# Performance work log

Hardware: AMD Instinct MI355X
Metric: run time of the kernel (lower is better)

The kernel has to match this reference:

```python
import jax, jax.numpy as jnp
import numpy as np

EPS = 1e-5  # BatchNorm eps (torch default)


def point_sample(feat, points):
    """Bilinear sample feat [B,C,Hf,Wf] at points [B,K,2] (x,y in [0,1]),
    matching F.grid_sample(2*p-1, mode='bilinear', padding_mode='zeros',
    align_corners=False)."""
    B, C, Hf, Wf = feat.shape
    x = points[..., 0] * Wf - 0.5  # [B,K] pixel coords
    y = points[..., 1] * Hf - 0.5
    x0f = jnp.floor(x); y0f = jnp.floor(y)
    wx = (x - x0f)[:, None, :]  # [B,1,K]
    wy = (y - y0f)[:, None, :]
    x0 = x0f.astype(jnp.int32); y0 = y0f.astype(jnp.int32)
    flat = feat.reshape(B, C, Hf * Wf)

    def gather(xi, yi):
        valid = ((xi >= 0) & (xi < Wf) & (yi >= 0) & (yi < Hf))[:, None, :]
        lin = jnp.clip(yi, 0, Hf - 1) * Wf + jnp.clip(xi, 0, Wf - 1)  # [B,K]
        idx = jnp.broadcast_to(lin[:, None, :], (B, C, lin.shape[1]))
        return jnp.take_along_axis(flat, idx, axis=2) * valid

    v00 = gather(x0, y0)
    v10 = gather(x0 + 1, y0)
    v01 = gather(x0, y0 + 1)
    v11 = gather(x0 + 1, y0 + 1)
    return (v00 * (1 - wx) * (1 - wy) + v10 * wx * (1 - wy)
            + v01 * (1 - wx) * wy + v11 * wx * wy)


def bn(x, g, b, m, v):
    # eval-mode BatchNorm1d over channel dim of [B,C,K]
    scale = (g / jnp.sqrt(v + EPS))[None, :, None]
    return (x - m[None, :, None]) * scale + b[None, :, None]


def setup_inputs() -> dict:
    key = jax.random.key(0)
    ks = jax.random.split(key, 20)
    B, H, W = 8, 512, 512
    Cf = 256
    d = {
        'uncertainty_map': jax.random.normal(ks[0], (B, 1, H, W), jnp.float32),
        'prev_mask': jax.random.uniform(ks[1], (B, 1, H, W), jnp.float32),
        'enc_f': jax.random.normal(ks[2], (B, Cf, 128, 128), jnp.float32),
        'w1': jax.random.normal(ks[3], (256, Cf + 1), jnp.float32) * 0.05,
        'b1': jax.random.normal(ks[4], (256,), jnp.float32) * 0.05,
        'g1': jnp.ones((256,), jnp.float32),
        'be1': jnp.zeros((256,), jnp.float32),
        'm1': jax.random.normal(ks[5], (256,), jnp.float32) * 0.1,
        'v1': jax.random.uniform(ks[6], (256,), jnp.float32) + 0.5,
        'w2': jax.random.normal(ks[7], (256, 256), jnp.float32) * 0.05,
        'b2': jax.random.normal(ks[8], (256,), jnp.float32) * 0.05,
        'g2': jnp.ones((256,), jnp.float32),
        'be2': jnp.zeros((256,), jnp.float32),
        'm2': jax.random.normal(ks[9], (256,), jnp.float32) * 0.1,
        'v2': jax.random.uniform(ks[10], (256,), jnp.float32) + 0.5,
        'w3': jax.random.normal(ks[11], (1, 256), jnp.float32) * 0.05,
        'b3': jax.random.normal(ks[12], (1,), jnp.float32) * 0.05,
    }
    return d


def reference(uncertainty_map, prev_mask, enc_f,
              w1, b1, g1, be1, m1, v1,
              w2, b2, g2, be2, m2, v2,
              w3, b3):
    B, C, H, W = prev_mask.shape
    K = H * W // 10
    # K least-uncertain points (topk largest=False)
    _, idx = jax.lax.top_k(-uncertainty_map.reshape(B, -1), K)  # [B,K] int32
    col = (idx % W).astype(jnp.float32)
    row = (idx // W).astype(jnp.float32)
    points = jnp.stack([(col + 0.5) / W, (row + 0.5) / H], axis=-1)  # [B,K,2]

    coarse = point_sample(prev_mask, points)  # [B,1,K]
    fine = point_sample(enc_f, points)        # [B,Cf,K]
    h = jnp.concatenate([coarse, fine], axis=1)  # [B,Cf+1,K]

    h = jax.nn.relu(bn(jnp.einsum('oc,bck->bok', w1, h) + b1[None, :, None], g1, be1, m1, v1))
    h = jax.nn.relu(bn(jnp.einsum('oc,bck->bok', w2, h) + b2[None, :, None], g2, be2, m2, v2))
    refined = jax.nn.sigmoid(jnp.einsum('oc,bck->bok', w3, h) + b3[None, :, None])  # [B,1,K]

    flat = prev_mask.reshape(B, C, H * W)
    bi = jnp.arange(B)[:, None, None]
    ci = jnp.arange(C)[None, :, None]
    out = flat.at[bi, ci, idx[:, None, :]].set(jnp.broadcast_to(refined, (B, C, K)))
    return out.reshape(B, C, H, W)
```

## Files before the change

kernel.cpp:

```cpp
#include <hip/hip_runtime.h>
#include <hip/hip_bf16.h>

#define HW_IMG 262144
#define KSEL   26214
#define NB     8
#define CF     256
#define LDW1   288
#define LDACT  296
#define GBLK   410
#define MBLK   205
#define NPTS_PAD 26240

#define ACOL(c) ((c) ^ ((((c) >> 6) & 3) << 4))

typedef short    short8 __attribute__((ext_vector_type(8)));
typedef float    f32x4  __attribute__((ext_vector_type(4)));
typedef unsigned u32x2  __attribute__((ext_vector_type(2)));
typedef unsigned short u16x4 __attribute__((ext_vector_type(4)));

__device__ __forceinline__ unsigned f2key(float f){
    unsigned u = __builtin_bit_cast(unsigned, f);
    return (u & 0x80000000u) ? ~u : (u | 0x80000000u);
}
__device__ __forceinline__ unsigned short f2bf(float f){
    unsigned u = __builtin_bit_cast(unsigned, f);
    u = u + 0x7FFFu + ((u >> 16) & 1u);
    return (unsigned short)(u >> 16);
}
__device__ __forceinline__ float bf2f(unsigned short s){
    unsigned u = ((unsigned)s) << 16;
    return __builtin_bit_cast(float, u);
}

__global__ __launch_bounds__(256) void k_prep(
    const float* __restrict__ w1, const float* __restrict__ w2,
    const float* __restrict__ b1, const float* __restrict__ g1, const float* __restrict__ be1,
    const float* __restrict__ m1, const float* __restrict__ v1,
    const float* __restrict__ b2, const float* __restrict__ g2, const float* __restrict__ be2,
    const float* __restrict__ m2, const float* __restrict__ v2,
    unsigned short* __restrict__ w1p, unsigned short* __restrict__ w2p,
    float* __restrict__ c1, float* __restrict__ c2)
{
    int tid = blockIdx.x * 256 + threadIdx.x;
    if (tid < 256 * LDW1) {
        int o = tid / LDW1, k = tid % LDW1;
        float scale = g1[o] * rsqrtf(v1[o] + 1e-5f);
        float val = 0.f;
        if (k < 256) val = w1[o * 257 + k + 1];
        else if (k == 256) val = w1[o * 257];
        w1p[tid] = f2bf(val * scale);
        if (k == 0) c1[o] = (b1[o] - m1[o]) * scale + be1[o];
    } else {
        int t2 = tid - 256 * LDW1;
        if (t2 < 65536) {
            int o = t2 >> 8;
            float scale = g2[o] * rsqrtf(v2[o] + 1e-5f);
            w2p[t2] = f2bf(w2[t2] * scale);
            if ((t2 & 255) == 0) c2[o] = (b2[o] - m2[o]) * scale + be2[o];
        }
    }
}

__global__ __launch_bounds__(256) void k_transpose(
    const float* __restrict__ enc, unsigned short* __restrict__ encT)
{
    __shared__ __align__(16) unsigned short tile[64][72];
    int b = blockIdx.z;
    int pixbase = blockIdx.x * 64;
    int chbase  = blockIdx.y * 64;
    int t = threadIdx.x;
    int pix = t & 63, cg = t >> 6;
    const float* src = enc + (size_t)b * CF * 16384;
#pragma unroll
    for (int i = 0; i < 16; i++) {
        int c = chbase + cg * 16 + i;
        tile[pix][cg * 16 + i] = f2bf(src[(size_t)c * 16384 + pixbase + pix]);
    }
    __syncthreads();
    unsigned short* dst = encT + (size_t)b * 16384 * CF;
#pragma unroll
    for (int pass = 0; pass < 4; pass++) {
        int pl = pass * 16 + (t >> 4);
        int c4 = (t & 15) * 4;
        *(u16x4*)(dst + (size_t)(pixbase + pl) * CF + chbase + c4) = *(const u16x4*)&tile[pl][c4];
    }
}


__global__ __launch_bounds__(256) void k_histA(const float* __restrict__ unc, unsigned* __restrict__ hist)
{
    __shared__ unsigned lh[4][4096];
    int b = blockIdx.y, t = threadIdx.x;
    int wv = t >> 6;
    for (int i = t; i < 4 * 4096; i += 256) ((unsigned*)lh)[i] = 0;
    __syncthreads();
    const float4* src = (const float4*)(unc + (size_t)b * HW_IMG + blockIdx.x * 4096);
    unsigned* mine = lh[wv];
#pragma unroll
    for (int j = 0; j < 4; j++) {
        float4 v = src[j * 256 + t];
        atomicAdd(&mine[f2key(v.x) >> 20], 1u);
        atomicAdd(&mine[f2key(v.y) >> 20], 1u);
        atomicAdd(&mine[f2key(v.z) >> 20], 1u);
        atomicAdd(&mine[f2key(v.w) >> 20], 1u);
    }
    __syncthreads();
    unsigned* gh = hist + (size_t)b * 4096;
    for (int i = t; i < 4096; i += 256) {
        unsigned c = lh[0][i] + lh[1][i] + lh[2][i] + lh[3][i];
        if (c) atomicAdd(&gh[i], c);
    }
}

__global__ __launch_bounds__(256) void k_histB(const float* __restrict__ unc,
    const unsigned* __restrict__ meta, unsigned* __restrict__ hist)
{
    __shared__ unsigned lh[4096];
    int b = blockIdx.y, t = threadIdx.x;
    unsigned binA = meta[b * 8 + 0];
    for (int i = t; i < 4096; i += 256) lh[i] = 0;
    __syncthreads();
    const float4* src = (const float4*)(unc + (size_t)b * HW_IMG + blockIdx.x * 4096);
#pragma unroll
    for (int j = 0; j < 4; j++) {
        float4 v = src[j * 256 + t];
        unsigned k;
        k = f2key(v.x); if ((k >> 20) == binA) atomicAdd(&lh[(k >> 8) & 0xFFFu], 1u);
        k = f2key(v.y); if ((k >> 20) == binA) atomicAdd(&lh[(k >> 8) & 0xFFFu], 1u);
        k = f2key(v.z); if ((k >> 20) == binA) atomicAdd(&lh[(k >> 8) & 0xFFFu], 1u);
        k = f2key(v.w); if ((k >> 20) == binA) atomicAdd(&lh[(k >> 8) & 0xFFFu], 1u);
    }
    __syncthreads();
    unsigned* gh = hist + (size_t)b * 4096;
    for (int i = t; i < 4096; i += 256) { unsigned c = lh[i]; if (c) atomicAdd(&gh[i], c); }
}

__global__ __launch_bounds__(256) void k_histC(const float* __restrict__ unc,
    const unsigned* __restrict__ meta, unsigned* __restrict__ hist)
{
    __shared__ unsigned lh[256];
    int b = blockIdx.y, t = threadIdx.x;
    unsigned pre24 = (meta[b * 8 + 0] << 12) | meta[b * 8 + 2];
    lh[t] = 0;
    __syncthreads();
    const float4* src = (const float4*)(unc + (size_t)b * HW_IMG + blockIdx.x * 4096);
#pragma unroll
    for (int j = 0; j < 4; j++) {
        float4 v = src[j * 256 + t];
        unsigned k;
        k = f2key(v.x); if ((k >> 8) == pre24) atomicAdd(&lh[k & 0xFFu], 1u);
        k = f2key(v.y); if ((k >> 8) == pre24) atomicAdd(&lh[k & 0xFFu], 1u);
        k = f2key(v.z); if ((k >> 8) == pre24) atomicAdd(&lh[k & 0xFFu], 1u);
        k = f2key(v.w); if ((k >> 8) == pre24) atomicAdd(&lh[k & 0xFFu], 1u);
    }
    __syncthreads();
    unsigned* gh = hist + (size_t)b * 4096;
    unsigned c = lh[t];
    if (c) atomicAdd(&gh[t], c);
}

__global__ __launch_bounds__(256) void k_find(const unsigned* __restrict__ hist,
    unsigned* __restrict__ meta, int per, int stage)
{
    int b = blockIdx.x, t = threadIdx.x;
    const unsigned* h = hist + (size_t)b * 4096;
    unsigned base = (stage == 0) ? 0u : meta[b * 8 + 2 * stage - 1];
    __shared__ unsigned seg[256], pref[256];
    unsigned s = 0;
    for (int i = 0; i < per; i++) s += h[t * per + i];
    seg[t] = s;
    __syncthreads();
    if (t == 0) { unsigned c = base; for (int i = 0; i < 256; i++) { pref[i] = c; c += seg[i]; } }
    __syncthreads();
    if (pref[t] < KSEL && KSEL <= pref[t] + seg[t]) {
        unsigned c = pref[t];
        for (int i = 0; i < per; i++) {
            unsigned cnt = h[t * per + i];
            if (c + cnt >= KSEL) {
                unsigned bin = (unsigned)(t * per + i);
                meta[b * 8 + 2 * stage] = bin;
                meta[b * 8 + 2 * stage + 1] = c;
                if (stage == 2)
                    meta[b * 8 + 6] = (meta[b * 8 + 0] << 20) | (meta[b * 8 + 2] << 8) | bin;
                break;
            }
            c += cnt;
        }
    }
}

__global__ __launch_bounds__(256) void k_count(const float* __restrict__ unc,
    const unsigned* __restrict__ meta, unsigned* __restrict__ cntL, unsigned* __restrict__ cntE)
{
    int b = blockIdx.y, blk = blockIdx.x, t = threadIdx.x;
    unsigned pivot = meta[b * 8 + 6];
    const float4* src = (const float4*)(unc + (size_t)b * HW_IMG + blk * 1024);
    float4 v = src[t];
    unsigned k0 = f2key(v.x), k1 = f2key(v.y), k2 = f2key(v.z), k3 = f2key(v.w);
    unsigned cl = (k0 < pivot) + (k1 < pivot) + (k2 < pivot) + (k3 < pivot);
    unsigned ce = (k0 == pivot) + (k1 == pivot) + (k2 == pivot) + (k3 == pivot);
    __shared__ unsigned rl[256], re[256];
    rl[t] = cl; re[t] = ce; __syncthreads();
    for (int s = 128; s > 0; s >>= 1) { if (t < s) { rl[t] += rl[t + s]; re[t] += re[t + s]; } __syncthreads(); }
    if (t == 0) { cntL[b * 256 + blk] = rl[0]; cntE[b * 256 + blk] = re[0]; }
}

__global__ void k_scan(const unsigned* __restrict__ cntL, const unsigned* __restrict__ cntE,
                       unsigned* __restrict__ offL, unsigned* __restrict__ offE)
{
    int b = blockIdx.x;
    if (threadIdx.x == 0) {
        unsigned c = 0;
        for (int i = 0; i < 256; i++) { offL[b * 256 + i] = c; c += cntL[b * 256 + i]; }
        c = 0;
        for (int i = 0; i < 256; i++) { offE[b * 256 + i] = c; c += cntE[b * 256 + i]; }
    }
}

__global__ __launch_bounds__(256) void k_emit(const float* __restrict__ unc,
    const unsigned* __restrict__ meta, const unsigned* __restrict__ offL,
    const unsigned* __restrict__ offE, unsigned* __restrict__ sel)
{
    int b = blockIdx.y, blk = blockIdx.x, t = threadIdx.x;
    unsigned pivot = meta[b * 8 + 6], cless = meta[b * 8 + 5], r = KSEL - cless;
    int base = blk * 1024 + t * 4;
    const float4* src = (const float4*)(unc + (size_t)b * HW_IMG + blk * 1024);
    float4 v = src[t];
    unsigned key[4] = { f2key(v.x), f2key(v.y), f2key(v.z), f2key(v.w) };
    unsigned cl = 0, ce = 0;
#pragma unroll
    for (int j = 0; j < 4; j++) { cl += (key[j] < pivot); ce += (key[j] == pivot); }
    __shared__ unsigned sL[256], sE[256];
    sL[t] = cl; sE[t] = ce; __syncthreads();
    for (int off = 1; off < 256; off <<= 1) {
        unsigned aL = (t >= off) ? sL[t - off] : 0u;
        unsigned aE = (t >= off) ? sE[t - off] : 0u;
        __syncthreads();
        sL[t] += aL; sE[t] += aE;
        __syncthreads();
    }
    unsigned posL = offL[b * 256 + blk] + sL[t] - cl;
    unsigned posE = offE[b * 256 + blk] + sE[t] - ce;
    unsigned* sb = sel + (size_t)b * KSEL;
#pragma unroll
    for (int j = 0; j < 4; j++) {
        if (key[j] < pivot) { sb[posL++] = (unsigned)(base + j); }
        else if (key[j] == pivot) { if (posE < r) sb[cless + posE] = (unsigned)(base + j); posE++; }
    }
}

__global__ __launch_bounds__(256) void k_gather(
    const unsigned* __restrict__ sel, const unsigned short* __restrict__ encT,
    unsigned short* __restrict__ gout)
{
    int wg = blockIdx.x;
    int b  = wg & 7;
    int pbase = (wg >> 3) * 64;
    int t = threadIdx.x;
    const unsigned* selb = sel + (size_t)b * KSEL;

    int wv2 = t >> 6, l2 = t & 63;
    int g = l2 >> 2, sub = l2 & 3;
    int p = wv2 * 16 + g;
    int gi = pbase + p; if (gi >= KSEL) gi = KSEL - 1;
    unsigned id = selb[gi];
    int col = id & 511, row = (int)(id >> 9);
    float xf = (col - 1.5f) * 0.25f;
    float yf = (row - 1.5f) * 0.25f;
    float x0f = floorf(xf), y0f = floorf(yf);
    int x0 = (int)x0f, y0 = (int)y0f;
    float wx = xf - x0f, wy = yf - y0f;
    float wxa = (x0 >= 0) ? (1.f - wx) : 0.f;
    float wxb = (x0 <= 126) ? wx : 0.f;
    float wya = (y0 >= 0) ? (1.f - wy) : 0.f;
    float wyb = (y0 <= 126) ? wy : 0.f;
    int xc0 = x0 < 0 ? 0 : x0;
    int xc1 = (x0 + 1 > 127) ? 127 : x0 + 1;
    int yc0 = y0 < 0 ? 0 : y0;
    int yc1 = (y0 + 1 > 127) ? 127 : y0 + 1;
    float w00 = wxa * wya, w10 = wxb * wya, w01 = wxa * wyb, w11 = wxb * wyb;
    const unsigned short* bb = encT + (size_t)b * 16384 * CF;
    const unsigned short* p00 = bb + (size_t)(yc0 * 128 + xc0) * CF + sub * 8;
    const unsigned short* p10 = bb + (size_t)(yc0 * 128 + xc1) * CF + sub * 8;
    const unsigned short* p01 = bb + (size_t)(yc1 * 128 + xc0) * CF + sub * 8;
    const unsigned short* p11 = bb + (size_t)(yc1 * 128 + xc1) * CF + sub * 8;
    unsigned short* dst = gout + ((size_t)b * NPTS_PAD + pbase + p) * CF + sub * 8;
#pragma unroll 4
    for (int ch = 0; ch < 8; ch++) {
        int off = ch * 32;
        short8 va = *(const short8*)(p00 + off);
        short8 vb = *(const short8*)(p10 + off);
        short8 vc = *(const short8*)(p01 + off);
        short8 vd = *(const short8*)(p11 + off);
        short8 rr;
#pragma unroll
        for (int j = 0; j < 8; j++) {
            float f = w00 * bf2f((unsigned short)va[j]) + w10 * bf2f((unsigned short)vb[j])
                    + w01 * bf2f((unsigned short)vc[j]) + w11 * bf2f((unsigned short)vd[j]);
            rr[j] = (short)f2bf(f);
        }
        *(short8*)(dst + off) = rr;
    }
}

__global__ __launch_bounds__(512, 4) void k_mlp(
    const unsigned* __restrict__ sel, const float* __restrict__ prev,
    const unsigned short* __restrict__ gout,
    const unsigned short* __restrict__ w1p, const unsigned short* __restrict__ w2p,
    const float* __restrict__ c1, const float* __restrict__ c2,
    const float* __restrict__ w3, const float* __restrict__ b3,
    float* __restrict__ out)
{
    __shared__ __align__(16) unsigned short act[128][LDACT];
    __shared__ float sPart[8][128];

    int wg = blockIdx.x;
    int b  = wg & 7;
    int pbase = (wg >> 3) * 128;
    int npts = KSEL - pbase; if (npts > 128) npts = 128;
    int t = threadIdx.x;
    const unsigned* selb = sel + (size_t)b * KSEL;

    const unsigned short* src = gout + ((size_t)b * NPTS_PAD + pbase) * CF;
#pragma unroll
    for (int i = 0; i < 8; i++) {
        int e = i * 4096 + t * 8;
        short8 v = *(const short8*)(src + e);
        int pp = e >> 8, c = e & 255;
        *(short8*)&act[pp][ACOL(c)] = v;
    }
    if (t < 128) {
        int gi = pbase + t; if (gi >= KSEL) gi = KSEL - 1;
        unsigned id = selb[gi];
        float cv = prev[(size_t)b * HW_IMG + id];
        short8 z = {0,0,0,0,0,0,0,0};
        short8 c8 = z; c8[0] = (short)f2bf(cv);
        *(short8*)&act[t][256] = c8;
        *(short8*)&act[t][264] = z;
        *(short8*)&act[t][272] = z;
        *(short8*)&act[t][280] = z;
    }
    __syncthreads();

    int w = t >> 6, l = t & 63;
    int lr = l & 15, lk = l >> 4;
    f32x4 acc[2][8];
#pragma unroll
    for (int m = 0; m < 2; m++)
#pragma unroll
        for (int n = 0; n < 8; n++) acc[m][n] = (f32x4){0.f, 0.f, 0.f, 0.f};

#pragma unroll
    for (int kk = 0; kk < 9; kk++) {
        int k0 = kk * 32 + lk * 8;
        int k0s = ACOL(k0);
        short8 afr[2], bfr[8];
#pragma unroll
        for (int m = 0; m < 2; m++)
            afr[m] = *(const short8*)(w1p + (size_t)(w * 32 + m * 16 + lr) * LDW1 + k0);
#pragma unroll
        for (int n = 0; n < 8; n++)
            bfr[n] = *(const short8*)&act[n * 16 + lr][k0s];
#pragma unroll
        for (int m = 0; m < 2; m++)
#pragma unroll
            for (int n = 0; n < 8; n++)
                acc[m][n] = __builtin_amdgcn_mfma_f32_16x16x32_bf16(afr[m], bfr[n], acc[m][n], 0, 0, 0);
    }
    __syncthreads();

#pragma unroll
    for (int m = 0; m < 2; m++) {
        int chb = w * 32 + m * 16 + lk * 4;
        int chbs = ACOL(chb);
        float c0 = c1[chb], cA = c1[chb + 1], cB = c1[chb + 2], cC = c1[chb + 3];
#pragma unroll
        for (int n = 0; n < 8; n++) {
            int p = n * 16 + lr;
            float v0 = fmaxf(acc[m][n][0] + c0, 0.f);
            float v1 = fmaxf(acc[m][n][1] + cA, 0.f);
            float v2 = fmaxf(acc[m][n][2] + cB, 0.f);
            float v3 = fmaxf(acc[m][n][3] + cC, 0.f);
            u32x2 pk;
            pk[0] = (unsigned)f2bf(v0) | ((unsigned)f2bf(v1) << 16);
            pk[1] = (unsigned)f2bf(v2) | ((unsigned)f2bf(v3) << 16);
            *(u32x2*)&act[p][chbs] = pk;
        }
    }
    __syncthreads();

#pragma unroll
    for (int m = 0; m < 2; m++)
#pragma unroll
        for (int n = 0; n < 8; n++) acc[m][n] = (f32x4){0.f, 0.f, 0.f, 0.f};
#pragma unroll
    for (int kk = 0; kk < 8; kk++) {
        int k0 = kk * 32 + lk * 8;
        int k0s = ACOL(k0);
        short8 afr[2], bfr[8];
#pragma unroll
        for (int m = 0; m < 2; m++)
            afr[m] = *(const short8*)(w2p + (size_t)(w * 32 + m * 16 + lr) * 256 + k0);
#pragma unroll
        for (int n = 0; n < 8; n++)
            bfr[n] = *(const short8*)&act[n * 16 + lr][k0s];
#pragma unroll
        for (int m = 0; m < 2; m++)
#pragma unroll
            for (int n = 0; n < 8; n++)
                acc[m][n] = __builtin_amdgcn_mfma_f32_16x16x32_bf16(afr[m], bfr[n], acc[m][n], 0, 0, 0);
    }

    float part[8] = {0.f, 0.f, 0.f, 0.f, 0.f, 0.f, 0.f, 0.f};
#pragma unroll
    for (int m = 0; m < 2; m++) {
        int chb = w * 32 + m * 16 + lk * 4;
#pragma unroll
        for (int r = 0; r < 4; r++) {
            float wr = w3[chb + r];
            float cr = c2[chb + r];
#pragma unroll
            for (int n = 0; n < 8; n++)
                part[n] += wr * fmaxf(acc[m][n][r] + cr, 0.f);
        }
    }
#pragma unroll
    for (int n = 0; n < 8; n++) {
        part[n] += __shfl_xor(part[n], 16);
        part[n] += __shfl_xor(part[n], 32);
    }
    if (lk == 0) {
#pragma unroll
        for (int n = 0; n < 8; n++) sPart[w][n * 16 + lr] = part[n];
    }
    __syncthreads();
    if (t < 128 && t < npts) {
        float tot = b3[0];
#pragma unroll
        for (int ww = 0; ww < 8; ww++) tot += sPart[ww][t];
        float refined = 1.f / (1.f + __expf(-tot));
        unsigned id = selb[pbase + t];
        out[(size_t)b * HW_IMG + id] = refined;
    }
}

extern "C" void kernel_launch(void* const* d_in, const int* in_sizes, int n_in,
                              void* d_out, int out_size, void* d_ws, size_t ws_size,
                              hipStream_t stream)
{
    (void)in_sizes; (void)n_in; (void)out_size; (void)ws_size;
    const float* unc  = (const float*)d_in[0];
    const float* prev = (const float*)d_in[1];
    const float* enc  = (const float*)d_in[2];
    const float* w1   = (const float*)d_in[3];
    const float* b1   = (const float*)d_in[4];
    const float* g1   = (const float*)d_in[5];
    const float* be1  = (const float*)d_in[6];
    const float* m1   = (const float*)d_in[7];
    const float* v1   = (const float*)d_in[8];
    const float* w2   = (const float*)d_in[9];
    const float* b2   = (const float*)d_in[10];
    const float* g2   = (const float*)d_in[11];
    const float* be2  = (const float*)d_in[12];
    const float* m2   = (const float*)d_in[13];
    const float* v2   = (const float*)d_in[14];
    const float* w3   = (const float*)d_in[15];
    const float* b3   = (const float*)d_in[16];
    float* out = (float*)d_out;

    char* ws = (char*)d_ws;
    size_t off = 0;
    auto alloc = [&](size_t bytes) { size_t o = off; off += (bytes + 255) & ~(size_t)255; return o; };
    size_t o_encT = alloc((size_t)NB * 16384 * CF * 2);
    size_t o_gout = alloc((size_t)NB * NPTS_PAD * CF * 2);
    size_t o_w1p  = alloc((size_t)256 * LDW1 * 2);
    size_t o_w2p  = alloc((size_t)256 * 256 * 2);
    size_t o_c1   = alloc(256 * 4);
    size_t o_c2   = alloc(256 * 4);
    size_t o_hist = alloc((size_t)3 * NB * 4096 * 4);
    size_t o_meta = alloc(NB * 8 * 4);
    size_t o_cntL = alloc(NB * 256 * 4);
    size_t o_cntE = alloc(NB * 256 * 4);
    size_t o_offL = alloc(NB * 256 * 4);
    size_t o_offE = alloc(NB * 256 * 4);
    size_t o_sel  = alloc((size_t)NB * KSEL * 4);

    unsigned short* encT = (unsigned short*)(ws + o_encT);
    unsigned short* goutp= (unsigned short*)(ws + o_gout);
    unsigned short* w1p  = (unsigned short*)(ws + o_w1p);
    unsigned short* w2p  = (unsigned short*)(ws + o_w2p);
    float* c1p = (float*)(ws + o_c1);
    float* c2p = (float*)(ws + o_c2);
    unsigned* histA = (unsigned*)(ws + o_hist);
    unsigned* histB = histA + (size_t)NB * 4096;
    unsigned* histC = histB + (size_t)NB * 4096;
    unsigned* meta  = (unsigned*)(ws + o_meta);
    unsigned* cntL  = (unsigned*)(ws + o_cntL);
    unsigned* cntE  = (unsigned*)(ws + o_cntE);
    unsigned* offL  = (unsigned*)(ws + o_offL);
    unsigned* offE  = (unsigned*)(ws + o_offE);
    unsigned* sel   = (unsigned*)(ws + o_sel);

    hipMemsetAsync(ws + o_hist, 0, (size_t)3 * NB * 4096 * 4, stream);
    hipMemcpyAsync(d_out, (const void*)prev, (size_t)NB * HW_IMG * 4, hipMemcpyDeviceToDevice, stream);

    k_prep<<<544, 256, 0, stream>>>(w1, w2, b1, g1, be1, m1, v1, b2, g2, be2, m2, v2,
                                    w1p, w2p, c1p, c2p);
    k_transpose<<<dim3(256, 4, NB), 256, 0, stream>>>(enc, encT);

    k_histA<<<dim3(64, NB), 256, 0, stream>>>(unc, histA);
    k_find <<<NB, 256, 0, stream>>>(histA, meta, 16, 0);
    k_histB<<<dim3(64, NB), 256, 0, stream>>>(unc, meta, histB);
    k_find <<<NB, 256, 0, stream>>>(histB, meta, 16, 1);
    k_histC<<<dim3(64, NB), 256, 0, stream>>>(unc, meta, histC);
    k_find <<<NB, 256, 0, stream>>>(histC, meta, 1, 2);
    k_count<<<dim3(256, NB), 256, 0, stream>>>(unc, meta, cntL, cntE);
    k_scan <<<NB, 64, 0, stream>>>(cntL, cntE, offL, offE);
    k_emit <<<dim3(256, NB), 256, 0, stream>>>(unc, meta, offL, offE, sel);

    k_gather<<<GBLK * NB, 256, 0, stream>>>(sel, encT, goutp);
    k_mlp   <<<MBLK * NB, 512, 0, stream>>>(sel, prev, goutp, w1p, w2p,
                                            c1p, c2p, w3, b3, out);
}
```

Measured before the change: 234.3 us.

## Fold coarse channel into epilogue FMA, flatten grids batch-interleaved, add nontemporal hints

The coarse mask channel is no longer padded into a ninth K-slice of the first GEMM. It is applied as a rank-1 FP32 term (w1c0 * coarse) in the layer-1 epilogue, which cuts one MFMA k-iteration and shrinks the shared activation tile and weight stride. All multi-dimensional grids become 1D with the batch index in the low bits, so neighbouring workgroups spread across batches. Nontemporal loads and stores are added on streaming data. The coarse term now stays in FP32 instead of BF16, a slight numerical difference.

```diff
diff --git a/kernel.cpp b/kernel.cpp
--- a/kernel.cpp
+++ b/kernel.cpp
@@ -5,8 +5,7 @@
 #define KSEL   26214
 #define NB     8
 #define CF     256
-#define LDW1   288
-#define LDACT  296
+#define LDACT  264
 #define GBLK   410
 #define MBLK   205
 #define NPTS_PAD 26240
@@ -39,25 +38,23 @@
     const float* __restrict__ b2, const float* __restrict__ g2, const float* __restrict__ be2,
     const float* __restrict__ m2, const float* __restrict__ v2,
     unsigned short* __restrict__ w1p, unsigned short* __restrict__ w2p,
-    float* __restrict__ c1, float* __restrict__ c2)
+    float* __restrict__ c1, float* __restrict__ c2, float* __restrict__ w1c0)
 {
     int tid = blockIdx.x * 256 + threadIdx.x;
-    if (tid < 256 * LDW1) {
-        int o = tid / LDW1, k = tid % LDW1;
+    if (tid < 65536) {
+        int o = tid >> 8, k = tid & 255;
         float scale = g1[o] * rsqrtf(v1[o] + 1e-5f);
-        float val = 0.f;
-        if (k < 256) val = w1[o * 257 + k + 1];
-        else if (k == 256) val = w1[o * 257];
-        w1p[tid] = f2bf(val * scale);
-        if (k == 0) c1[o] = (b1[o] - m1[o]) * scale + be1[o];
+        w1p[tid] = f2bf(w1[o * 257 + k + 1] * scale);
+        if (k == 0) {
+            c1[o] = (b1[o] - m1[o]) * scale + be1[o];
+            w1c0[o] = w1[o * 257] * scale;
+        }
     } else {
-        int t2 = tid - 256 * LDW1;
-        if (t2 < 65536) {
-            int o = t2 >> 8;
-            float scale = g2[o] * rsqrtf(v2[o] + 1e-5f);
-            w2p[t2] = f2bf(w2[t2] * scale);
-            if ((t2 & 255) == 0) c2[o] = (b2[o] - m2[o]) * scale + be2[o];
-        }
+        int t2 = tid - 65536;
+        int o = t2 >> 8;
+        float scale = g2[o] * rsqrtf(v2[o] + 1e-5f);
+        w2p[t2] = f2bf(w2[t2] * scale);
+        if ((t2 & 255) == 0) c2[o] = (b2[o] - m2[o]) * scale + be2[o];
     }
 }
 
@@ -65,16 +62,19 @@
     const float* __restrict__ enc, unsigned short* __restrict__ encT)
 {
     __shared__ __align__(16) unsigned short tile[64][72];
-    int b = blockIdx.z;
-    int pixbase = blockIdx.x * 64;
-    int chbase  = blockIdx.y * 64;
+    int wg = blockIdx.x;
+    int b = wg & 7;
+    int r = wg >> 3;
+    int pixbase = (r & 255) * 64;
+    int chbase  = (r >> 8) * 64;
     int t = threadIdx.x;
     int pix = t & 63, cg = t >> 6;
     const float* src = enc + (size_t)b * CF * 16384;
 #pragma unroll
     for (int i = 0; i < 16; i++) {
         int c = chbase + cg * 16 + i;
-        tile[pix][cg * 16 + i] = f2bf(src[(size_t)c * 16384 + pixbase + pix]);
+        float v = __builtin_nontemporal_load(&src[(size_t)c * 16384 + pixbase + pix]);
+        tile[pix][cg * 16 + i] = f2bf(v);
     }
     __syncthreads();
     unsigned short* dst = encT + (size_t)b * 16384 * CF;
@@ -90,11 +90,12 @@
 __global__ __launch_bounds__(256) void k_histA(const float* __restrict__ unc, unsigned* __restrict__ hist)
 {
     __shared__ unsigned lh[4][4096];
-    int b = blockIdx.y, t = threadIdx.x;
+    int wg = blockIdx.x;
+    int b = wg & 7, x = wg >> 3, t = threadIdx.x;
     int wv = t >> 6;
     for (int i = t; i < 4 * 4096; i += 256) ((unsigned*)lh)[i] = 0;
     __syncthreads();
-    const float4* src = (const float4*)(unc + (size_t)b * HW_IMG + blockIdx.x * 4096);
+    const float4* src = (const float4*)(unc + (size_t)b * HW_IMG + x * 4096);
     unsigned* mine = lh[wv];
 #pragma unroll
     for (int j = 0; j < 4; j++) {
@@ -116,11 +117,12 @@
     const unsigned* __restrict__ meta, unsigned* __restrict__ hist)
 {
     __shared__ unsigned lh[4096];
-    int b = blockIdx.y, t = threadIdx.x;
+    int wg = blockIdx.x;
+    int b = wg & 7, x = wg >> 3, t = threadIdx.x;
     unsigned binA = meta[b * 8 + 0];
     for (int i = t; i < 4096; i += 256) lh[i] = 0;
     __syncthreads();
-    const float4* src = (const float4*)(unc + (size_t)b * HW_IMG + blockIdx.x * 4096);
+    const float4* src = (const float4*)(unc + (size_t)b * HW_IMG + x * 4096);
 #pragma unroll
     for (int j = 0; j < 4; j++) {
         float4 v = src[j * 256 + t];
@@ -139,11 +141,12 @@
     const unsigned* __restrict__ meta, unsigned* __restrict__ hist)
 {
     __shared__ unsigned lh[256];
-    int b = blockIdx.y, t = threadIdx.x;
+    int wg = blockIdx.x;
+    int b = wg & 7, x = wg >> 3, t = threadIdx.x;
     unsigned pre24 = (meta[b * 8 + 0] << 12) | meta[b * 8 + 2];
     lh[t] = 0;
     __syncthreads();
-    const float4* src = (const float4*)(unc + (size_t)b * HW_IMG + blockIdx.x * 4096);
+    const float4* src = (const float4*)(unc + (size_t)b * HW_IMG + x * 4096);
 #pragma unroll
     for (int j = 0; j < 4; j++) {
         float4 v = src[j * 256 + t];
@@ -192,7 +195,8 @@
 __global__ __launch_bounds__(256) void k_count(const float* __restrict__ unc,
     const unsigned* __restrict__ meta, unsigned* __restrict__ cntL, unsigned* __restrict__ cntE)
 {
-    int b = blockIdx.y, blk = blockIdx.x, t = threadIdx.x;
+    int wg = blockIdx.x;
+    int b = wg & 7, blk = wg >> 3, t = threadIdx.x;
     unsigned pivot = meta[b * 8 + 6];
     const float4* src = (const float4*)(unc + (size_t)b * HW_IMG + blk * 1024);
     float4 v = src[t];
@@ -221,7 +225,8 @@
     const unsigned* __restrict__ meta, const unsigned* __restrict__ offL,
     const unsigned* __restrict__ offE, unsigned* __restrict__ sel)
 {
-    int b = blockIdx.y, blk = blockIdx.x, t = threadIdx.x;
+    int wg = blockIdx.x;
+    int b = wg & 7, blk = wg >> 3, t = threadIdx.x;
     unsigned pivot = meta[b * 8 + 6], cless = meta[b * 8 + 5], r = KSEL - cless;
     int base = blk * 1024 + t * 4;
     const float4* src = (const float4*)(unc + (size_t)b * HW_IMG + blk * 1024);
@@ -299,7 +304,7 @@
                     + w01 * bf2f((unsigned short)vc[j]) + w11 * bf2f((unsigned short)vd[j]);
             rr[j] = (short)f2bf(f);
         }
-        *(short8*)(dst + off) = rr;
+        __builtin_nontemporal_store(rr, (short8*)(dst + off));
     }
 }
 
@@ -309,10 +314,11 @@
     const unsigned short* __restrict__ w1p, const unsigned short* __restrict__ w2p,
     const float* __restrict__ c1, const float* __restrict__ c2,
     const float* __restrict__ w3, const float* __restrict__ b3,
-    float* __restrict__ out)
+    const float* __restrict__ w1c0, float* __restrict__ out)
 {
     __shared__ __align__(16) unsigned short act[128][LDACT];
     __shared__ float sPart[8][128];
+    __shared__ float sCoarse[128];
 
     int wg = blockIdx.x;
     int b  = wg & 7;
@@ -325,20 +331,14 @@
 #pragma unroll
     for (int i = 0; i < 8; i++) {
         int e = i * 4096 + t * 8;
-        short8 v = *(const short8*)(src + e);
+        short8 v = __builtin_nontemporal_load((const short8*)(src + e));
         int pp = e >> 8, c = e & 255;
         *(short8*)&act[pp][ACOL(c)] = v;
     }
     if (t < 128) {
         int gi = pbase + t; if (gi >= KSEL) gi = KSEL - 1;
         unsigned id = selb[gi];
-        float cv = prev[(size_t)b * HW_IMG + id];
-        short8 z = {0,0,0,0,0,0,0,0};
-        short8 c8 = z; c8[0] = (short)f2bf(cv);
-        *(short8*)&act[t][256] = c8;
-        *(short8*)&act[t][264] = z;
-        *(short8*)&act[t][272] = z;
-        *(short8*)&act[t][280] = z;
+        sCoarse[t] = __builtin_nontemporal_load(&prev[(size_t)b * HW_IMG + id]);
     }
     __syncthreads();
 
@@ -351,13 +351,13 @@
         for (int n = 0; n < 8; n++) acc[m][n] = (f32x4){0.f, 0.f, 0.f, 0.f};
 
 #pragma unroll
-    for (int kk = 0; kk < 9; kk++) {
+    for (int kk = 0; kk < 8; kk++) {
         int k0 = kk * 32 + lk * 8;
         int k0s = ACOL(k0);
         short8 afr[2], bfr[8];
 #pragma unroll
         for (int m = 0; m < 2; m++)
-            afr[m] = *(const short8*)(w1p + (size_t)(w * 32 + m * 16 + lr) * LDW1 + k0);
+            afr[m] = *(const short8*)(w1p + (size_t)(w * 32 + m * 16 + lr) * 256 + k0);
 #pragma unroll
         for (int n = 0; n < 8; n++)
             bfr[n] = *(const short8*)&act[n * 16 + lr][k0s];
@@ -374,13 +374,15 @@
         int chb = w * 32 + m * 16 + lk * 4;
         int chbs = ACOL(chb);
         float c0 = c1[chb], cA = c1[chb + 1], cB = c1[chb + 2], cC = c1[chb + 3];
+        float q0 = w1c0[chb], qA = w1c0[chb + 1], qB = w1c0[chb + 2], qC = w1c0[chb + 3];
 #pragma unroll
         for (int n = 0; n < 8; n++) {
             int p = n * 16 + lr;
-            float v0 = fmaxf(acc[m][n][0] + c0, 0.f);
-            float v1 = fmaxf(acc[m][n][1] + cA, 0.f);
-            float v2 = fmaxf(acc[m][n][2] + cB, 0.f);
-            float v3 = fmaxf(acc[m][n][3] + cC, 0.f);
+            float cv = sCoarse[p];
+            float v0 = fmaxf(acc[m][n][0] + c0 + q0 * cv, 0.f);
+            float v1 = fmaxf(acc[m][n][1] + cA + qA * cv, 0.f);
+            float v2 = fmaxf(acc[m][n][2] + cB + qB * cv, 0.f);
+            float v3 = fmaxf(acc[m][n][3] + cC + qC * cv, 0.f);
             u32x2 pk;
             pk[0] = (unsigned)f2bf(v0) | ((unsigned)f2bf(v1) << 16);
             pk[1] = (unsigned)f2bf(v2) | ((unsigned)f2bf(v3) << 16);
@@ -440,7 +442,7 @@
         for (int ww = 0; ww < 8; ww++) tot += sPart[ww][t];
         float refined = 1.f / (1.f + __expf(-tot));
         unsigned id = selb[pbase + t];
-        out[(size_t)b * HW_IMG + id] = refined;
+        __builtin_nontemporal_store(refined, &out[(size_t)b * HW_IMG + id]);
     }
 }
 
@@ -473,10 +475,11 @@
     auto alloc = [&](size_t bytes) { size_t o = off; off += (bytes + 255) & ~(size_t)255; return o; };
     size_t o_encT = alloc((size_t)NB * 16384 * CF * 2);
     size_t o_gout = alloc((size_t)NB * NPTS_PAD * CF * 2);
-    size_t o_w1p  = alloc((size_t)256 * LDW1 * 2);
+    size_t o_w1p  = alloc((size_t)256 * 256 * 2);
     size_t o_w2p  = alloc((size_t)256 * 256 * 2);
     size_t o_c1   = alloc(256 * 4);
     size_t o_c2   = alloc(256 * 4);
+    size_t o_w1c0 = alloc(256 * 4);
     size_t o_hist = alloc((size_t)3 * NB * 4096 * 4);
     size_t o_meta = alloc(NB * 8 * 4);
     size_t o_cntL = alloc(NB * 256 * 4);
@@ -491,6 +494,7 @@
     unsigned short* w2p  = (unsigned short*)(ws + o_w2p);
     float* c1p = (float*)(ws + o_c1);
     float* c2p = (float*)(ws + o_c2);
+    float* w1c0p = (float*)(ws + o_w1c0);
     unsigned* histA = (unsigned*)(ws + o_hist);
     unsigned* histB = histA + (size_t)NB * 4096;
     unsigned* histC = histB + (size_t)NB * 4096;
@@ -504,21 +508,21 @@
     hipMemsetAsync(ws + o_hist, 0, (size_t)3 * NB * 4096 * 4, stream);
     hipMemcpyAsync(d_out, (const void*)prev, (size_t)NB * HW_IMG * 4, hipMemcpyDeviceToDevice, stream);
 
-    k_prep<<<544, 256, 0, stream>>>(w1, w2, b1, g1, be1, m1, v1, b2, g2, be2, m2, v2,
-                                    w1p, w2p, c1p, c2p);
-    k_transpose<<<dim3(256, 4, NB), 256, 0, stream>>>(enc, encT);
-
-    k_histA<<<dim3(64, NB), 256, 0, stream>>>(unc, histA);
+    k_prep<<<512, 256, 0, stream>>>(w1, w2, b1, g1, be1, m1, v1, b2, g2, be2, m2, v2,
+                                    w1p, w2p, c1p, c2p, w1c0p);
+    k_transpose<<<8192, 256, 0, stream>>>(enc, encT);
+
+    k_histA<<<512, 256, 0, stream>>>(unc, histA);
     k_find <<<NB, 256, 0, stream>>>(histA, meta, 16, 0);
-    k_histB<<<dim3(64, NB), 256, 0, stream>>>(unc, meta, histB);
+    k_histB<<<512, 256, 0, stream>>>(unc, meta, histB);
     k_find <<<NB, 256, 0, stream>>>(histB, meta, 16, 1);
-    k_histC<<<dim3(64, NB), 256, 0, stream>>>(unc, meta, histC);
+    k_histC<<<512, 256, 0, stream>>>(unc, meta, histC);
     k_find <<<NB, 256, 0, stream>>>(histC, meta, 1, 2);
-    k_count<<<dim3(256, NB), 256, 0, stream>>>(unc, meta, cntL, cntE);
+    k_count<<<2048, 256, 0, stream>>>(unc, meta, cntL, cntE);
     k_scan <<<NB, 64, 0, stream>>>(cntL, cntE, offL, offE);
-    k_emit <<<dim3(256, NB), 256, 0, stream>>>(unc, meta, offL, offE, sel);
+    k_emit <<<2048, 256, 0, stream>>>(unc, meta, offL, offE, sel);
 
     k_gather<<<GBLK * NB, 256, 0, stream>>>(sel, encT, goutp);
     k_mlp   <<<MBLK * NB, 512, 0, stream>>>(sel, prev, goutp, w1p, w2p,
-                                            c1p, c2p, w3, b3, out);
-}
+                                            c1p, c2p, w3, b3, w1c0p, out);
+}
```

After: 218.6 us. -6.7%, faster.
